# Performance work log

Measured on AMD Instinct MI355X. Metric: run time of the kernel, lower is better.

Reference implementation:

```python
import jax, jax.numpy as jnp
import numpy as np

B, S, D, H = 2, 2048, 1024, 16
DK = D // H

def setup_inputs() -> dict:
    key = jax.random.key(0)
    ks = jax.random.split(key, 11)
    s = 1.0 / np.sqrt(D)
    return {
        "q": jax.random.normal(ks[0], (B, S, D), jnp.float32),
        "k": jax.random.normal(ks[1], (B, S, D), jnp.float32),
        "v": jax.random.normal(ks[2], (B, S, D), jnp.float32),
        "Wq": jax.random.normal(ks[3], (D, D), jnp.float32) * s,
        "bq": jax.random.normal(ks[4], (D,), jnp.float32) * s,
        "Wk": jax.random.normal(ks[5], (D, D), jnp.float32) * s,
        "bk": jax.random.normal(ks[6], (D,), jnp.float32) * s,
        "Wv": jax.random.normal(ks[7], (D, D), jnp.float32) * s,
        "bv": jax.random.normal(ks[8], (D,), jnp.float32) * s,
        "Wo": jax.random.normal(ks[9], (D, D), jnp.float32) * s,
        "bo": jax.random.normal(ks[10], (D,), jnp.float32) * s,
    }

def reference(q, k, v, Wq, bq, Wk, bk, Wv, bv, Wo, bo):
    # Linear projections, then split into heads: [B,S,D] -> [B,H,S,DK]
    def heads(x, W, b):
        y = x @ W.T + b
        return y.reshape(B, S, H, DK).transpose(0, 2, 1, 3)
    qh = heads(q, Wq, bq)
    kh = heads(k, Wk, bk)
    vh = heads(v, Wv, bv)
    scores = jnp.einsum('bhsd,bhtd->bhst', qh, kh) / jnp.sqrt(jnp.float32(DK))
    attn = jax.nn.softmax(scores, axis=-1)
    out = jnp.einsum('bhst,bhtd->bhsd', attn, vh)  # [B,H,S,DK]
    out = out.transpose(0, 2, 1, 3).reshape(B, S, D)
    return out @ Wo.T + bo
```

## Files before the change

### kernel.cpp

```cpp
#include <hip/hip_runtime.h>
#include <stdint.h>

#define B_  2
#define S_  2048
#define D_  1024
#define H_  16
#define DK_ 64

typedef unsigned short u16;
typedef __attribute__((ext_vector_type(8))) __bf16 bf16x8;
typedef __attribute__((ext_vector_type(4))) float f32x4;
typedef __attribute__((ext_vector_type(16))) float f32x16;
typedef __attribute__((ext_vector_type(4))) short short4v;
typedef __attribute__((ext_vector_type(8))) short short8v;

static __device__ __forceinline__ u16 f2bf(float f) {
    union { float f; uint32_t u; } v; v.f = f;
    return (u16)((v.u + 0x7fffu + ((v.u >> 16) & 1u)) >> 16);
}
static __device__ __forceinline__ uint32_t pk2bf(float x, float y) {
    return (uint32_t)f2bf(x) | ((uint32_t)f2bf(y) << 16);
}
static __device__ __forceinline__ uint32_t cvtpk_bf16(float lo, float hi) {
    uint32_t r; asm("v_cvt_pk_bf16_f32 %0, %1, %2" : "=v"(r) : "v"(lo), "v"(hi));
    return r;
}
static __device__ __forceinline__ float exp2f_fast(float x) {
    float r; asm("v_exp_f32 %0, %1" : "=v"(r) : "v"(x)); return r;
}

#define GLOAD16(gp, lp) \
    __builtin_amdgcn_global_load_lds((const __attribute__((address_space(1))) void*)(gp), \
                                     (__attribute__((address_space(3))) void*)(lp), 16, 0, 0)

static __device__ __forceinline__ int swz(int lin) { return lin ^ ((lin >> 3) & 7); }
static __device__ __forceinline__ int swz2(int lin) {
    return lin ^ ((lin >> 3) & 7) ^ ((lin >> 6) & 3);
}

static __device__ __forceinline__ int xcd_swz(int bid, int cpx) {
    return (bid & 7) * cpx + (bid >> 3);
}

__global__ __launch_bounds__(256) void cast_all_kernel(
        const float* __restrict__ q, const float* __restrict__ k, const float* __restrict__ v,
        const float* __restrict__ Wq, const float* __restrict__ Wk,
        const float* __restrict__ Wv, const float* __restrict__ Wo,
        u16* __restrict__ qb, u16* __restrict__ kb, u16* __restrict__ vb,
        u16* __restrict__ Wqb, u16* __restrict__ Wkb, u16* __restrict__ Wvb,
        u16* __restrict__ Wob) {
    int blk = blockIdx.x;
    const float* src; u16* dst; int off;
    if (blk < 2048)      { src = q;  dst = qb;  off = blk; }
    else if (blk < 4096) { src = k;  dst = kb;  off = blk - 2048; }
    else if (blk < 6144) { src = v;  dst = vb;  off = blk - 4096; }
    else if (blk < 6656) { src = Wq; dst = Wqb; off = blk - 6144; }
    else if (blk < 7168) { src = Wk; dst = Wkb; off = blk - 6656; }
    else if (blk < 7680) { src = Wv; dst = Wvb; off = blk - 7168; }
    else                 { src = Wo; dst = Wob; off = blk - 7680; }
    int i = (off * 256 + threadIdx.x) * 8;
    float4 a = *(const float4*)(src + i);
    float4 b = *(const float4*)(src + i + 4);
    uint4 r;
    r.x = pk2bf(a.x, a.y); r.y = pk2bf(a.z, a.w);
    r.z = pk2bf(b.x, b.y); r.w = pk2bf(b.z, b.w);
    *(uint4*)(void*)(dst + i) = r;
}

__device__ __forceinline__ void gemm128_compute(
        const u16* __restrict__ X, const u16* __restrict__ W,
        int m0, int n0, u16* lds, f32x4 acc[4][4]) {
    const int tid = threadIdx.x, lane = tid & 63, w = tid >> 6;
    const int wm = w >> 1, wn = w & 1;
    u16* As = lds;
    u16* Bs = lds + 8192;

    auto stage = [&](int bi, int kt) {
#pragma unroll
        for (int r = 0; r < 2; ++r) {
            int s = tid + (r << 8);
            int lin = s ^ ((s >> 3) & 7);
            int row = lin >> 2, ch = lin & 3;
            GLOAD16(X + (size_t)(m0 + row) * 1024 + (kt << 5) + (ch << 3),
                    (char*)(As + bi * 4096) + ((r << 8) + (w << 6)) * 16);
            GLOAD16(W + (size_t)(n0 + row) * 1024 + (kt << 5) + (ch << 3),
                    (char*)(Bs + bi * 4096) + ((r << 8) + (w << 6)) * 16);
        }
    };

    stage(0, 0);
    asm volatile("s_waitcnt vmcnt(0)" ::: "memory");
    __syncthreads();
#pragma unroll 1
    for (int kt = 0; kt < 32; ++kt) {
        const int cur = kt & 1;
        if (kt < 31) stage(cur ^ 1, kt + 1);
        const char* Ab = (const char*)(As + cur * 4096);
        const char* Bb = (const char*)(Bs + cur * 4096);
        bf16x8 a[4], b[4];
#pragma unroll
        for (int f = 0; f < 4; ++f) {
            int rowa = wm * 64 + f * 16 + (lane & 15);
            a[f] = *(const bf16x8*)(Ab + swz(rowa * 4 + (lane >> 4)) * 16);
            int rowb = wn * 64 + f * 16 + (lane & 15);
            b[f] = *(const bf16x8*)(Bb + swz(rowb * 4 + (lane >> 4)) * 16);
        }
#pragma unroll
        for (int fm = 0; fm < 4; ++fm)
#pragma unroll
            for (int fn = 0; fn < 4; ++fn)
                acc[fm][fn] = __builtin_amdgcn_mfma_f32_16x16x32_bf16(
                    a[fm], b[fn], acc[fm][fn], 0, 0, 0);
        __syncthreads();
    }
}

__device__ __forceinline__ void stage_half(const u16* __restrict__ src,
        int R0, int kt, u16* dst, int tid) {
#pragma unroll
    for (int r = 0; r < 2; ++r) {
        int s = tid + (r << 9);
        int lin = s ^ ((s >> 3) & 7);
        int row = lin >> 3, ch = lin & 7;
        GLOAD16(src + (size_t)(R0 + row) * 1024 + (kt << 6) + (ch << 3),
                (char*)dst + ((r << 9) + ((tid >> 6) << 6)) * 16);
    }
}

#define VM4  asm volatile("s_waitcnt vmcnt(4)" ::: "memory")
#define VM0  asm volatile("s_waitcnt vmcnt(0)" ::: "memory")

#define PHASE(QQ, MP, LOADB, STAGE_STMT, VM_STMT)                                \
    {                                                                            \
        bf16x8 afr[2][2];                                                        \
        if (LOADB) {                                                             \
            _Pragma("unroll") for (int fn = 0; fn < 4; ++fn)                     \
            _Pragma("unroll") for (int ks = 0; ks < 2; ++ks) {                   \
                int lin = (brow0 + fn * 16 + (lane & 15)) * 8 + ks * 4 + (lane >> 4); \
                bfr[fn][ks] = *(const bf16x8*)(Bhb[QQ] + swz(lin) * 16);         \
            }                                                                    \
        }                                                                        \
        _Pragma("unroll") for (int fo = 0; fo < 2; ++fo)                         \
        _Pragma("unroll") for (int ks = 0; ks < 2; ++ks) {                       \
            int lin = ((MP) * 32 + fo * 16 + (lane & 15)) * 8 + ks * 4 + (lane >> 4); \
            afr[fo][ks] = *(const bf16x8*)(Ahb[QQ] + swz(lin) * 16);             \
        }                                                                        \
        STAGE_STMT;                                                              \
        VM_STMT;                                                                 \
        __builtin_amdgcn_s_barrier();                                            \
        __builtin_amdgcn_sched_barrier(0);                                       \
        __builtin_amdgcn_s_setprio(1);                                           \
        _Pragma("unroll") for (int fo = 0; fo < 2; ++fo)                         \
        _Pragma("unroll") for (int ks = 0; ks < 2; ++ks)                         \
        _Pragma("unroll") for (int fn = 0; fn < 4; ++fn)                         \
            acc[(MP) * 2 + fo][fn] = __builtin_amdgcn_mfma_f32_16x16x32_bf16(    \
                afr[fo][ks], bfr[fn][ks], acc[(MP) * 2 + fo][fn], 0, 0, 0);      \
        __builtin_amdgcn_s_setprio(0);                                           \
        __builtin_amdgcn_s_barrier();                                            \
        __builtin_amdgcn_sched_barrier(0);                                       \
    }

__global__ __launch_bounds__(512, 2) void qkv256_kernel(
        const u16* __restrict__ qX, const u16* __restrict__ kX, const u16* __restrict__ vX,
        const u16* __restrict__ Wq, const u16* __restrict__ Wk, const u16* __restrict__ Wv,
        const float* __restrict__ bq, const float* __restrict__ bk, const float* __restrict__ bv,
        u16* __restrict__ qo, u16* __restrict__ ko, u16* __restrict__ vt) {
    __shared__ __align__(16) u16 lds[65536];
    const int tid = threadIdx.x, lane = tid & 63, w = tid >> 6;
    const int wm = w >> 2, wn = w & 3;
    const int lg = xcd_swz(blockIdx.x, 24);
    const int which = lg >> 6;
    const int rem = lg & 63;
    const int n0 = (rem >> 4) << 8;
    const int m0 = (rem & 15) << 8;
    const u16* X = which == 0 ? qX : (which == 1 ? kX : vX);
    const u16* W = which == 0 ? Wq : (which == 1 ? Wk : Wv);
    const float* bias = which == 0 ? bq : (which == 1 ? bk : bv);

    u16* Abase = lds;
    u16* Bbase = lds + 32768;

    stage_half(X, m0,        0, Abase + 0,             tid);
    stage_half(X, m0 + 128,  0, Abase + 8192,          tid);
    stage_half(W, n0,        0, Bbase + 0,             tid);
    stage_half(W, n0 + 128,  0, Bbase + 8192,          tid);
    stage_half(W, n0,        1, Bbase + 16384,         tid);
    stage_half(W, n0 + 128,  1, Bbase + 16384 + 8192,  tid);
    VM4;
    __builtin_amdgcn_s_barrier();
    __builtin_amdgcn_sched_barrier(0);

    f32x4 acc[8][4] = {};
    bf16x8 bfr[4][2];
    const char* Ahb[2] = { (const char*)(Abase + wm * 8192),
                           (const char*)(Abase + 16384 + wm * 8192) };
    const char* Bhb[2] = { (const char*)(Bbase + (wn >> 1) * 8192),
                           (const char*)(Bbase + 16384 + (wn >> 1) * 8192) };
    const int brow0 = (wn & 1) * 64;

#pragma unroll 1
    for (int i = 0; i < 8; ++i) {
        const int t0 = 2 * i, t1 = 2 * i + 1;
        const bool nl = (i < 7);
        PHASE(0, 0, true,  stage_half(X, m0,       t1,     Abase + 16384,        tid), (void)0);
        PHASE(0, 1, false, stage_half(X, m0 + 128, t1,     Abase + 16384 + 8192, tid), (void)0);
        PHASE(0, 2, false, if (nl) stage_half(W, n0,       t0 + 2, Bbase + 0,    tid), (void)0);
        PHASE(0, 3, false, if (nl) stage_half(W, n0 + 128, t0 + 2, Bbase + 8192, tid),
              if (nl) { VM4; } else { VM0; });
        PHASE(1, 0, true,  if (nl) stage_half(X, m0,       t0 + 2, Abase + 0,    tid), (void)0);
        PHASE(1, 1, false, if (nl) stage_half(X, m0 + 128, t0 + 2, Abase + 8192, tid), (void)0);
        PHASE(1, 2, false, if (nl) stage_half(W, n0,       t1 + 2, Bbase + 16384, tid), (void)0);
        PHASE(1, 3, false, if (nl) stage_half(W, n0 + 128, t1 + 2, Bbase + 16384 + 8192, tid),
              if (nl) { VM4; });
    }

    if (which < 2) {
        u16* out = which == 0 ? qo : ko;
        const float scale = which == 0 ? 0.1803368801111883f : 1.0f;
#pragma unroll
        for (int fn = 0; fn < 4; ++fn) {
            int n = n0 + wn * 64 + fn * 16 + (lane & 15);
            float bb = bias[n];
            int h = n >> 6, dk = n & 63;
#pragma unroll
            for (int fm = 0; fm < 8; ++fm)
#pragma unroll
                for (int j = 0; j < 4; ++j) {
                    int m = m0 + wm * 128 + fm * 16 + (lane >> 4) * 4 + j;
                    int b = m >> 11, s = m & 2047;
                    out[((size_t)(b * H_ + h) * S_ + s) * DK_ + dk] =
                        f2bf((acc[fm][fn][j] + bb) * scale);
                }
        }
    } else {
        __syncthreads();
        u16* wl = lds + w * 8192;
#pragma unroll
        for (int fn = 0; fn < 4; ++fn) {
            int dk = fn * 16 + (lane & 15);
            float bb = bias[n0 + wn * 64 + dk];
            int xr = (dk & 7) << 3;
#pragma unroll
            for (int fm = 0; fm < 8; ++fm) {
                int sl = fm * 16 + (lane >> 4) * 4;
                short4v p;
#pragma unroll
                for (int j = 0; j < 4; ++j) p[j] = (short)f2bf(acc[fm][fn][j] + bb);
                *(short4v*)(void*)&wl[dk * 128 + (sl ^ xr)] = p;
            }
        }
        int mrow = m0 + wm * 128;
        int b = mrow >> 11, sbase = mrow & 2047;
        int h = (n0 >> 6) + wn;
        u16* dst = vt + ((size_t)(b * H_ + h) * DK_) * S_ + sbase;
#pragma unroll
        for (int oc = 0; oc < 8; ++oc)
#pragma unroll
            for (int ic = 0; ic < 2; ++ic) {
                int dk = oc * 8 + (lane >> 3);
                int sc = ic * 8 + (lane & 7);
                short8v vv = *(const short8v*)(const void*)
                    &wl[dk * 128 + ((sc * 8) ^ ((dk & 7) << 3))];
                *(short8v*)(void*)(dst + (size_t)dk * S_ + sc * 8) = vv;
            }
    }
}

__global__ __launch_bounds__(256) void oproj_kernel(
        const u16* __restrict__ X, const u16* __restrict__ W,
        const float* __restrict__ bias, float* __restrict__ out) {
    __shared__ __align__(16) u16 lds[16384];
    const int bid = xcd_swz(blockIdx.x, 32);
    const int m0 = (bid >> 3) << 7;
    const int n0 = (bid & 7) << 7;
    f32x4 acc[4][4] = {};
    gemm128_compute(X, W, m0, n0, lds, acc);

    const int lane = threadIdx.x & 63, w = threadIdx.x >> 6;
    const int wm = w >> 1, wn = w & 1;
#pragma unroll
    for (int fn = 0; fn < 4; ++fn) {
        int n = n0 + wn * 64 + fn * 16 + (lane & 15);
        float bb = bias[n];
#pragma unroll
        for (int fm = 0; fm < 4; ++fm)
#pragma unroll
            for (int j = 0; j < 4; ++j) {
                int m = m0 + wm * 64 + fm * 16 + (lane >> 4) * 4 + j;
                out[(size_t)m * 1024 + n] = acc[fm][fn][j] + bb;
            }
    }
}

__global__ __launch_bounds__(256, 2) void attn_kernel(
        const u16* __restrict__ qh, const u16* __restrict__ kh,
        const u16* __restrict__ Vt, u16* __restrict__ ao) {
    __shared__ __align__(16) u16 Ks[4][4096];
    __shared__ __align__(16) u16 Vs[4][4096];

    const int tid = threadIdx.x, lane = tid & 63, w = tid >> 6;
    const int l31 = lane & 31, hh = lane >> 5;
    const int lg = xcd_swz(blockIdx.x, 64);
    const int bh = lg >> 4, qt = lg & 15;
    const u16* qg = qh + ((size_t)bh * S_ + qt * 128) * DK_;
    const u16* kg = kh + (size_t)bh * S_ * DK_;
    const u16* vg = Vt + (size_t)bh * DK_ * S_;

    const int lin0 = swz2(tid), lin1 = swz2(tid + 256);
    const u16* ksrc0 = kg + (lin0 >> 3) * 64 + ((lin0 & 7) << 3);
    const u16* ksrc1 = kg + (lin1 >> 3) * 64 + ((lin1 & 7) << 3);
    const u16* vsrc0 = vg + (size_t)(lin0 >> 3) * S_ + ((lin0 & 7) << 3);
    const u16* vsrc1 = vg + (size_t)(lin1 >> 3) * S_ + ((lin1 & 7) << 3);
    char* kdst0 = (char*)(&Ks[0][0]) + (w << 6) * 16;
    char* kdst1 = (char*)(&Ks[0][0]) + (256 + (w << 6)) * 16;
    char* vdst0 = (char*)(&Vs[0][0]) + (w << 6) * 16;
    char* vdst1 = (char*)(&Vs[0][0]) + (256 + (w << 6)) * 16;

    auto stageKV = [&](int slot, int kt) {
        const int sb = slot << 13;
        GLOAD16(ksrc0 + (kt << 12), kdst0 + sb);
        GLOAD16(ksrc1 + (kt << 12), kdst1 + sb);
        GLOAD16(vsrc0 + (kt << 6),  vdst0 + sb);
        GLOAD16(vsrc1 + (kt << 6),  vdst1 + sb);
    };

    int loff[2][4];
#pragma unroll
    for (int b = 0; b < 2; ++b)
#pragma unroll
        for (int c = 0; c < 4; ++c)
            loff[b][c] = swz2((b * 32 + l31) * 8 + c * 2 + hh) * 16;

    stageKV(0, 0);
    stageKV(1, 1);
    bf16x8 qf[4];
#pragma unroll
    for (int c = 0; c < 4; ++c)
        qf[c] = *(const bf16x8*)(qg + (size_t)(w * 32 + l31) * 64 + c * 16 + hh * 8);
    asm volatile("s_waitcnt vmcnt(0)" ::: "memory");
    __syncthreads();

    f32x16 acc[2] = {};
    float rs = 0.f;

#pragma unroll 1
    for (int i = 0; i < 32; ++i) {
        if (i < 30) stageKV((i + 2) & 3, i + 2);

        const char* Kb = (const char*)(&Ks[0][0]) + ((i & 3) << 13);
        f32x16 st[2] = {};
#pragma unroll
        for (int kb = 0; kb < 2; ++kb) {
            bf16x8 kf[4];
#pragma unroll
            for (int c = 0; c < 4; ++c)
                kf[c] = *(const bf16x8*)(Kb + loff[kb][c]);
            __builtin_amdgcn_s_setprio(1);
#pragma unroll
            for (int c = 0; c < 4; ++c)
                st[kb] = __builtin_amdgcn_mfma_f32_32x32x16_bf16(
                    kf[c], qf[c], st[kb], 0, 0, 0);
            __builtin_amdgcn_s_setprio(0);
        }

        bf16x8 pa[4];
#pragma unroll
        for (int c = 0; c < 4; ++c) {
            const int kb = c >> 1, o = (c & 1) * 8;
            float e0 = exp2f_fast(st[kb][o + 0]);
            float e1 = exp2f_fast(st[kb][o + 1]);
            float e2 = exp2f_fast(st[kb][o + 2]);
            float e3 = exp2f_fast(st[kb][o + 3]);
            float e4 = exp2f_fast(st[kb][o + 4]);
            float e5 = exp2f_fast(st[kb][o + 5]);
            float e6 = exp2f_fast(st[kb][o + 6]);
            float e7 = exp2f_fast(st[kb][o + 7]);
            rs += ((e0 + e1) + (e2 + e3)) + ((e4 + e5) + (e6 + e7));
            uint32_t u0 = cvtpk_bf16(e0, e1);
            uint32_t u1 = cvtpk_bf16(e2, e3);
            uint32_t u2 = cvtpk_bf16(e4, e5);
            uint32_t u3 = cvtpk_bf16(e6, e7);
            asm volatile("v_permlane32_swap_b32 %0, %1" : "+v"(u0), "+v"(u2));
            asm volatile("v_permlane32_swap_b32 %0, %1" : "+v"(u1), "+v"(u3));
            union { uint32_t u[4]; bf16x8 v; } pu;
            pu.u[0] = u0; pu.u[1] = u1; pu.u[2] = u2; pu.u[3] = u3;
            pa[c] = pu.v;
        }

        const char* Vb = (const char*)(&Vs[0][0]) + ((i & 3) << 13);
#pragma unroll
        for (int nb = 0; nb < 2; ++nb) {
            bf16x8 vf[4];
#pragma unroll
            for (int c = 0; c < 4; ++c)
                vf[c] = *(const bf16x8*)(Vb + loff[nb][c]);
            __builtin_amdgcn_s_setprio(1);
#pragma unroll
            for (int c = 0; c < 4; ++c)
                acc[nb] = __builtin_amdgcn_mfma_f32_32x32x16_bf16(
                    pa[c], vf[c], acc[nb], 0, 0, 0);
            __builtin_amdgcn_s_setprio(0);
        }

        if (i < 31) {
            if (i < 30) { asm volatile("s_waitcnt vmcnt(4)" ::: "memory"); }
            else        { asm volatile("s_waitcnt vmcnt(0)" ::: "memory"); }
            __builtin_amdgcn_s_barrier();
            __builtin_amdgcn_sched_barrier(0);
        }
    }

    rs += __shfl_xor(rs, 32);
    const int bb = bh >> 4, hd = bh & 15;
#pragma unroll
    for (int r = 0; r < 16; ++r) {
        int ql = (r & 3) + 8 * (r >> 2) + 4 * hh;
        float inv = 1.0f / __shfl(rs, ql);
        int srow = qt * 128 + w * 32 + ql;
#pragma unroll
        for (int nb = 0; nb < 2; ++nb) {
            int col = hd * 64 + nb * 32 + l31;
            ao[((size_t)bb * S_ + srow) * D_ + col] = f2bf(acc[nb][r] * inv);
        }
    }
}

extern "C" void kernel_launch(void* const* d_in, const int* in_sizes, int n_in,
                              void* d_out, int out_size, void* d_ws, size_t ws_size,
                              hipStream_t stream) {
    const float* q  = (const float*)d_in[0];
    const float* k  = (const float*)d_in[1];
    const float* v  = (const float*)d_in[2];
    const float* Wq = (const float*)d_in[3];
    const float* bq = (const float*)d_in[4];
    const float* Wk = (const float*)d_in[5];
    const float* bk = (const float*)d_in[6];
    const float* Wv = (const float*)d_in[7];
    const float* bv = (const float*)d_in[8];
    const float* Wo = (const float*)d_in[9];
    const float* bo = (const float*)d_in[10];

    char* ws = (char*)d_ws;
    u16* qb  = (u16*)(ws);
    u16* kb  = (u16*)(ws + (8u  << 20));
    u16* vb  = (u16*)(ws + (16u << 20));
    u16* Wqb = (u16*)(ws + (24u << 20));
    u16* Wkb = (u16*)(ws + (26u << 20));
    u16* Wvb = (u16*)(ws + (28u << 20));
    u16* Wob = (u16*)(ws + (30u << 20));
    u16* qhb = (u16*)(ws + (32u << 20));
    u16* khb = (u16*)(ws + (40u << 20));
    u16* Vtb = (u16*)(ws + (48u << 20));
    u16* aob = kb;

    cast_all_kernel<<<8192, 256, 0, stream>>>(q, k, v, Wq, Wk, Wv, Wo,
                                              qb, kb, vb, Wqb, Wkb, Wvb, Wob);

    qkv256_kernel<<<192, 512, 0, stream>>>(
        qb, kb, vb, Wqb, Wkb, Wvb, bq, bk, bv, qhb, khb, Vtb);

    attn_kernel<<<512, 256, 0, stream>>>(qhb, khb, Vtb, aob);

    oproj_kernel<<<256, 256, 0, stream>>>(aob, Wob, bo, (float*)d_out);
}
```

Measured before the change: 117.4 us.

## Load attention K/V directly from global memory and halve output-projection M tile

The attention kernel drops its LDS ring buffer and barriers for K/V. Each wave now loads its K and V fragments straight from global memory into registers every iteration, relying on L2/cache reuse across the four waves and removing LDS traffic and synchronisation. Separately, the output projection tile shrinks from 128x128 to 64x128 and the grid doubles to 512 blocks, for more parallelism. This trades more global/L2 traffic and register pressure in attention for less sync, and risks exposed global-load latency now that no software pipelining remains.

```diff
diff --git a/kernel.cpp b/kernel.cpp
--- a/kernel.cpp
+++ b/kernel.cpp
@@ -34,9 +34,6 @@
                                      (__attribute__((address_space(3))) void*)(lp), 16, 0, 0)
 
 static __device__ __forceinline__ int swz(int lin) { return lin ^ ((lin >> 3) & 7); }
-static __device__ __forceinline__ int swz2(int lin) {
-    return lin ^ ((lin >> 3) & 7) ^ ((lin >> 6) & 3);
-}
 
 static __device__ __forceinline__ int xcd_swz(int bid, int cpx) {
     return (bid & 7) * cpx + (bid >> 3);
@@ -65,54 +62,6 @@
     r.x = pk2bf(a.x, a.y); r.y = pk2bf(a.z, a.w);
     r.z = pk2bf(b.x, b.y); r.w = pk2bf(b.z, b.w);
     *(uint4*)(void*)(dst + i) = r;
-}
-
-__device__ __forceinline__ void gemm128_compute(
-        const u16* __restrict__ X, const u16* __restrict__ W,
-        int m0, int n0, u16* lds, f32x4 acc[4][4]) {
-    const int tid = threadIdx.x, lane = tid & 63, w = tid >> 6;
-    const int wm = w >> 1, wn = w & 1;
-    u16* As = lds;
-    u16* Bs = lds + 8192;
-
-    auto stage = [&](int bi, int kt) {
-#pragma unroll
-        for (int r = 0; r < 2; ++r) {
-            int s = tid + (r << 8);
-            int lin = s ^ ((s >> 3) & 7);
-            int row = lin >> 2, ch = lin & 3;
-            GLOAD16(X + (size_t)(m0 + row) * 1024 + (kt << 5) + (ch << 3),
-                    (char*)(As + bi * 4096) + ((r << 8) + (w << 6)) * 16);
-            GLOAD16(W + (size_t)(n0 + row) * 1024 + (kt << 5) + (ch << 3),
-                    (char*)(Bs + bi * 4096) + ((r << 8) + (w << 6)) * 16);
-        }
-    };
-
-    stage(0, 0);
-    asm volatile("s_waitcnt vmcnt(0)" ::: "memory");
-    __syncthreads();
-#pragma unroll 1
-    for (int kt = 0; kt < 32; ++kt) {
-        const int cur = kt & 1;
-        if (kt < 31) stage(cur ^ 1, kt + 1);
-        const char* Ab = (const char*)(As + cur * 4096);
-        const char* Bb = (const char*)(Bs + cur * 4096);
-        bf16x8 a[4], b[4];
-#pragma unroll
-        for (int f = 0; f < 4; ++f) {
-            int rowa = wm * 64 + f * 16 + (lane & 15);
-            a[f] = *(const bf16x8*)(Ab + swz(rowa * 4 + (lane >> 4)) * 16);
-            int rowb = wn * 64 + f * 16 + (lane & 15);
-            b[f] = *(const bf16x8*)(Bb + swz(rowb * 4 + (lane >> 4)) * 16);
-        }
-#pragma unroll
-        for (int fm = 0; fm < 4; ++fm)
-#pragma unroll
-            for (int fn = 0; fn < 4; ++fn)
-                acc[fm][fn] = __builtin_amdgcn_mfma_f32_16x16x32_bf16(
-                    a[fm], b[fn], acc[fm][fn], 0, 0, 0);
-        __syncthreads();
-    }
 }
 
 __device__ __forceinline__ void stage_half(const u16* __restrict__ src,
@@ -269,24 +218,71 @@
 __global__ __launch_bounds__(256) void oproj_kernel(
         const u16* __restrict__ X, const u16* __restrict__ W,
         const float* __restrict__ bias, float* __restrict__ out) {
-    __shared__ __align__(16) u16 lds[16384];
-    const int bid = xcd_swz(blockIdx.x, 32);
-    const int m0 = (bid >> 3) << 7;
+    __shared__ __align__(16) u16 lds[12288];
+    const int tid = threadIdx.x, lane = tid & 63, w = tid >> 6;
+    const int wm = w >> 1, wn = w & 1;
+    const int bid = xcd_swz(blockIdx.x, 64);
+    const int m0 = (bid >> 3) << 6;
     const int n0 = (bid & 7) << 7;
-    f32x4 acc[4][4] = {};
-    gemm128_compute(X, W, m0, n0, lds, acc);
-
-    const int lane = threadIdx.x & 63, w = threadIdx.x >> 6;
-    const int wm = w >> 1, wn = w & 1;
+    u16* As = lds;
+    u16* Bs = lds + 4096;
+
+    auto stage = [&](int bi, int kt) {
+        {
+            int lin = tid ^ ((tid >> 3) & 7);
+            int row = lin >> 2, ch = lin & 3;
+            GLOAD16(X + (size_t)(m0 + row) * 1024 + (kt << 5) + (ch << 3),
+                    (char*)(As + bi * 2048) + (w << 6) * 16);
+        }
+#pragma unroll
+        for (int r = 0; r < 2; ++r) {
+            int s = tid + (r << 8);
+            int lin = s ^ ((s >> 3) & 7);
+            int row = lin >> 2, ch = lin & 3;
+            GLOAD16(W + (size_t)(n0 + row) * 1024 + (kt << 5) + (ch << 3),
+                    (char*)(Bs + bi * 4096) + ((r << 8) + (w << 6)) * 16);
+        }
+    };
+
+    f32x4 acc[2][4] = {};
+    stage(0, 0);
+    asm volatile("s_waitcnt vmcnt(0)" ::: "memory");
+    __syncthreads();
+#pragma unroll 1
+    for (int kt = 0; kt < 32; ++kt) {
+        const int cur = kt & 1;
+        if (kt < 31) stage(cur ^ 1, kt + 1);
+        const char* Ab = (const char*)(As + cur * 2048);
+        const char* Bb = (const char*)(Bs + cur * 4096);
+        bf16x8 a[2], b[4];
+#pragma unroll
+        for (int f = 0; f < 2; ++f) {
+            int rowa = wm * 32 + f * 16 + (lane & 15);
+            a[f] = *(const bf16x8*)(Ab + swz(rowa * 4 + (lane >> 4)) * 16);
+        }
+#pragma unroll
+        for (int f = 0; f < 4; ++f) {
+            int rowb = wn * 64 + f * 16 + (lane & 15);
+            b[f] = *(const bf16x8*)(Bb + swz(rowb * 4 + (lane >> 4)) * 16);
+        }
+#pragma unroll
+        for (int fm = 0; fm < 2; ++fm)
+#pragma unroll
+            for (int fn = 0; fn < 4; ++fn)
+                acc[fm][fn] = __builtin_amdgcn_mfma_f32_16x16x32_bf16(
+                    a[fm], b[fn], acc[fm][fn], 0, 0, 0);
+        __syncthreads();
+    }
+
 #pragma unroll
     for (int fn = 0; fn < 4; ++fn) {
         int n = n0 + wn * 64 + fn * 16 + (lane & 15);
         float bb = bias[n];
 #pragma unroll
-        for (int fm = 0; fm < 4; ++fm)
+        for (int fm = 0; fm < 2; ++fm)
 #pragma unroll
             for (int j = 0; j < 4; ++j) {
-                int m = m0 + wm * 64 + fm * 16 + (lane >> 4) * 4 + j;
+                int m = m0 + wm * 32 + fm * 16 + (lane >> 4) * 4 + j;
                 out[(size_t)m * 1024 + n] = acc[fm][fn][j] + bb;
             }
     }
@@ -295,73 +291,51 @@
 __global__ __launch_bounds__(256, 2) void attn_kernel(
         const u16* __restrict__ qh, const u16* __restrict__ kh,
         const u16* __restrict__ Vt, u16* __restrict__ ao) {
-    __shared__ __align__(16) u16 Ks[4][4096];
-    __shared__ __align__(16) u16 Vs[4][4096];
-
     const int tid = threadIdx.x, lane = tid & 63, w = tid >> 6;
     const int l31 = lane & 31, hh = lane >> 5;
     const int lg = xcd_swz(blockIdx.x, 64);
     const int bh = lg >> 4, qt = lg & 15;
     const u16* qg = qh + ((size_t)bh * S_ + qt * 128) * DK_;
-    const u16* kg = kh + (size_t)bh * S_ * DK_;
-    const u16* vg = Vt + (size_t)bh * DK_ * S_;
-
-    const int lin0 = swz2(tid), lin1 = swz2(tid + 256);
-    const u16* ksrc0 = kg + (lin0 >> 3) * 64 + ((lin0 & 7) << 3);
-    const u16* ksrc1 = kg + (lin1 >> 3) * 64 + ((lin1 & 7) << 3);
-    const u16* vsrc0 = vg + (size_t)(lin0 >> 3) * S_ + ((lin0 & 7) << 3);
-    const u16* vsrc1 = vg + (size_t)(lin1 >> 3) * S_ + ((lin1 & 7) << 3);
-    char* kdst0 = (char*)(&Ks[0][0]) + (w << 6) * 16;
-    char* kdst1 = (char*)(&Ks[0][0]) + (256 + (w << 6)) * 16;
-    char* vdst0 = (char*)(&Vs[0][0]) + (w << 6) * 16;
-    char* vdst1 = (char*)(&Vs[0][0]) + (256 + (w << 6)) * 16;
-
-    auto stageKV = [&](int slot, int kt) {
-        const int sb = slot << 13;
-        GLOAD16(ksrc0 + (kt << 12), kdst0 + sb);
-        GLOAD16(ksrc1 + (kt << 12), kdst1 + sb);
-        GLOAD16(vsrc0 + (kt << 6),  vdst0 + sb);
-        GLOAD16(vsrc1 + (kt << 6),  vdst1 + sb);
-    };
-
-    int loff[2][4];
-#pragma unroll
-    for (int b = 0; b < 2; ++b)
-#pragma unroll
-        for (int c = 0; c < 4; ++c)
-            loff[b][c] = swz2((b * 32 + l31) * 8 + c * 2 + hh) * 16;
-
-    stageKV(0, 0);
-    stageKV(1, 1);
+
+    const u16* kbase = kh + (size_t)bh * S_ * DK_ + (size_t)l31 * 64 + hh * 8;
+    const u16* vbase = Vt + (size_t)bh * DK_ * S_ + (size_t)l31 * S_ + hh * 8;
+
     bf16x8 qf[4];
 #pragma unroll
     for (int c = 0; c < 4; ++c)
         qf[c] = *(const bf16x8*)(qg + (size_t)(w * 32 + l31) * 64 + c * 16 + hh * 8);
-    asm volatile("s_waitcnt vmcnt(0)" ::: "memory");
-    __syncthreads();
 
     f32x16 acc[2] = {};
     float rs = 0.f;
 
 #pragma unroll 1
-    for (int i = 0; i < 32; ++i) {
-        if (i < 30) stageKV((i + 2) & 3, i + 2);
-
-        const char* Kb = (const char*)(&Ks[0][0]) + ((i & 3) << 13);
+    for (int kt = 0; kt < 32; ++kt) {
+        const u16* kp = kbase + (size_t)(kt << 6) * 64;
+        bf16x8 kf[2][4];
+#pragma unroll
+        for (int kb = 0; kb < 2; ++kb)
+#pragma unroll
+            for (int c = 0; c < 4; ++c)
+                kf[kb][c] = *(const bf16x8*)(kp + (kb << 5) * 64 + (c << 4));
+
         f32x16 st[2] = {};
 #pragma unroll
         for (int kb = 0; kb < 2; ++kb) {
-            bf16x8 kf[4];
-#pragma unroll
-            for (int c = 0; c < 4; ++c)
-                kf[c] = *(const bf16x8*)(Kb + loff[kb][c]);
             __builtin_amdgcn_s_setprio(1);
 #pragma unroll
             for (int c = 0; c < 4; ++c)
                 st[kb] = __builtin_amdgcn_mfma_f32_32x32x16_bf16(
-                    kf[c], qf[c], st[kb], 0, 0, 0);
+                    kf[kb][c], qf[c], st[kb], 0, 0, 0);
             __builtin_amdgcn_s_setprio(0);
         }
+
+        const u16* vp = vbase + (kt << 6);
+        bf16x8 vf[2][4];
+#pragma unroll
+        for (int nb = 0; nb < 2; ++nb)
+#pragma unroll
+            for (int c = 0; c < 4; ++c)
+                vf[nb][c] = *(const bf16x8*)(vp + (size_t)(nb << 5) * S_ + (c << 4));
 
         bf16x8 pa[4];
 #pragma unroll
@@ -387,26 +361,14 @@
             pa[c] = pu.v;
         }
 
-        const char* Vb = (const char*)(&Vs[0][0]) + ((i & 3) << 13);
 #pragma unroll
         for (int nb = 0; nb < 2; ++nb) {
-            bf16x8 vf[4];
-#pragma unroll
-            for (int c = 0; c < 4; ++c)
-                vf[c] = *(const bf16x8*)(Vb + loff[nb][c]);
             __builtin_amdgcn_s_setprio(1);
 #pragma unroll
             for (int c = 0; c < 4; ++c)
                 acc[nb] = __builtin_amdgcn_mfma_f32_32x32x16_bf16(
-                    pa[c], vf[c], acc[nb], 0, 0, 0);
+                    pa[c], vf[nb][c], acc[nb], 0, 0, 0);
             __builtin_amdgcn_s_setprio(0);
-        }
-
-        if (i < 31) {
-            if (i < 30) { asm volatile("s_waitcnt vmcnt(4)" ::: "memory"); }
-            else        { asm volatile("s_waitcnt vmcnt(0)" ::: "memory"); }
-            __builtin_amdgcn_s_barrier();
-            __builtin_amdgcn_sched_barrier(0);
         }
     }
 
@@ -461,5 +423,5 @@
 
     attn_kernel<<<512, 256, 0, stream>>>(qhb, khb, Vtb, aob);
 
-    oproj_kernel<<<256, 256, 0, stream>>>(aob, Wob, bo, (float*)d_out);
-}
+    oproj_kernel<<<512, 256, 0, stream>>>(aob, Wob, bo, (float*)d_out);
+}
```

Measured after the change: 186.2 us. 58.7% more time.
